# Performance work log

Measured on AMD Instinct MI355X. Metric: run time of the kernel, lower is better.

Reference implementation:

```python
import jax, jax.numpy as jnp
import numpy as np
from jax import lax

C, H, W = 512, 4, 4          # channel, height, width (size=[512,4,4])
SPLIT, PRED = 4, 4
WC = W // SPLIT              # width of each chunk = 1
L = C * H * WC               # lstm_size = 2048
B = 16


def setup_inputs() -> dict:
    key = jax.random.key(0)
    ks = jax.random.split(key, 12)
    s = 0.02  # ~1/sqrt(L), keeps gates in a sane range
    def w(k, shape):
        return jax.random.normal(k, shape, jnp.float32) * s
    return {
        "x1": jax.random.normal(ks[0], (B, C, H, W), jnp.float32),
        "x2": jax.random.normal(ks[1], (B, C, H, W), jnp.float32),
        "enc_Wih": w(ks[2], (2, 4 * L, L)),
        "enc_Whh": w(ks[3], (2, 4 * L, L)),
        "enc_bih": w(ks[4], (2, 4 * L)),
        "enc_bhh": w(ks[5], (2, 4 * L)),
        "dec_Wih": w(ks[6], (2, 4 * L, L)),
        "dec_Whh": w(ks[7], (2, 4 * L, L)),
        "dec_bih": w(ks[8], (2, 4 * L)),
        "dec_bhh": w(ks[9], (2, 4 * L)),
        "conv_W": w(ks[10], (C, 2 * C)),
        "conv_b": w(ks[11], (C,)),
    }


def _lstm2(x, state, Wih, Whh, bih, bhh):
    """One time-step of a 2-layer torch-style LSTM. x: [B, L]."""
    h, c = state  # each [2, B, L]
    hs, cs = [], []
    inp = x
    for l in range(2):
        g = inp @ Wih[l].T + bih[l] + h[l] @ Whh[l].T + bhh[l]  # [B, 4L]
        i, f, gg, o = jnp.split(g, 4, axis=-1)  # torch gate order i,f,g,o
        cn = jax.nn.sigmoid(f) * c[l] + jax.nn.sigmoid(i) * jnp.tanh(gg)
        hn = jax.nn.sigmoid(o) * jnp.tanh(cn)
        hs.append(hn); cs.append(cn)
        inp = hn
    return inp, (jnp.stack(hs), jnp.stack(cs))


def _split_chunks(x, reverse_inside=False):
    # torch.stack(torch.split(x, WC, dim=3)).view(SPLIT, -1, 1, L)
    b = x.shape[0]
    a = x.reshape(b, C, H, SPLIT, WC)
    if reverse_inside:
        a = a[..., ::-1]  # flip(dims=[4]) on the stacked chunks
    a = jnp.moveaxis(a, 3, 0)  # [SPLIT, B, C, H, WC]
    return a.reshape(SPLIT, b, L)


def _assemble(chunks, b, flip_inside=False):
    # chunks: [K, B, L] -> image block [B, C, H, K*WC] (width-concat order = chunk order)
    k = chunks.shape[0]
    a = chunks.reshape(k, b, C, H, WC)
    if flip_inside:
        a = a[..., ::-1]  # per-chunk flip(dims=[3]) in the torch code
    a = jnp.transpose(a, (1, 2, 3, 0, 4))
    return a.reshape(b, C, H, k * WC)


def _forward(x1, x2, enc_Wih, enc_Whh, enc_bih, enc_bhh,
             dec_Wih, dec_Whh, dec_bih, dec_bhh, conv_W, conv_b):
    b = x1.shape[0]
    z = jnp.zeros((2, b, L), x1.dtype)
    init = (z, z)

    def enc_step(st, x):
        out, st2 = _lstm2(x, st, enc_Wih, enc_Whh, enc_bih, enc_bhh)
        return st2, out

    def dec_step(st, x):
        out, st2 = _lstm2(x, st, dec_Wih, dec_Whh, dec_bih, dec_bhh)
        return st2, out

    def dec_ar(x0, st, n):
        def step(carry, _):
            x, s = carry
            out, s2 = _lstm2(x, s, dec_Wih, dec_Whh, dec_bih, dec_bhh)
            return (out, s2), out
        _, outs = lax.scan(step, (x0, st), None, length=n)
        return outs  # [n, B, L]

    x1_split = _split_chunks(x1)
    x1_split_rev = _split_chunks(x1, reverse_inside=True)
    x2_split = _split_chunks(x2)
    x2_split_rev = _split_chunks(x2, reverse_inside=True)

    # encoder: forward over x2 chunks; backward over internally-flipped x1 chunks
    hidden_x2, _ = lax.scan(enc_step, init, x2_split)
    hidden_x1r, _ = lax.scan(enc_step, init, x1_split_rev[::-1])

    st1, outs1 = lax.scan(dec_step, hidden_x2, x1_split)
    de1 = outs1[-1]
    preds1 = dec_ar(de1, st1, PRED + SPLIT - 1)  # 7 steps
    extra1 = _assemble(jnp.concatenate([de1[None], preds1], 0), b)
    x1_full = jnp.concatenate([x1, extra1], axis=3)  # width 3*W

    # decoder branch 2: consume reversed x2 chunks from hidden_x1r, prepend outputs
    st2, outs2 = lax.scan(dec_step, hidden_x1r, x2_split_rev[::-1])
    de2 = outs2[-1]
    preds2 = dec_ar(de2, st2, PRED + SPLIT - 1)
    # each output is prepended, so the last prediction ends up at the front
    extra2 = _assemble(jnp.concatenate([preds2[::-1], de2[None]], 0), b, flip_inside=True)
    x2_full = jnp.concatenate([extra2, x2], axis=3)

    x1_parts = (x1_full[..., :W], x1_full[..., W:-W], x1_full[..., -W:])
    x2_parts = (x2_full[..., :W], x2_full[..., W:-W], x2_full[..., -W:])

    mid = jnp.concatenate([x1_parts[1], x2_parts[1]], axis=1)  # [B, 2C, H, W]
    out = jnp.einsum('oi,bihw->bohw', conv_W, mid) + conv_b[None, :, None, None]
    out = jax.nn.leaky_relu(out, 0.2)  # make_layers: 1x1 conv + LeakyReLU
    return out, x1_parts, x2_parts


def reference(x1, x2, enc_Wih, enc_Whh, enc_bih, enc_bhh,
              dec_Wih, dec_Whh, dec_bih, dec_bhh, conv_W, conv_b):
    out, p1, p2 = _forward(x1, x2, enc_Wih, enc_Whh, enc_bih, enc_bhh,
                           dec_Wih, dec_Whh, dec_bih, dec_bhh, conv_W, conv_b)
    return (out,) + p1 + p2
```

## Files before the change

kernel.cpp:

```cpp
#include <hip/hip_runtime.h>
#include <cstdint>
#include <cstddef>


typedef __attribute__((ext_vector_type(8))) short short8;
typedef __attribute__((ext_vector_type(4))) short short4v;
typedef __attribute__((ext_vector_type(4))) float f32x4;

#define NBATCH 16
#define MAT_B   16777216ull
#define WSCALE  64.0f
#define INVWS   (1.0f / 64.0f)

__device__ __forceinline__ short f2bf(float f) {
    union { float f; unsigned u; } c; c.f = f;
    unsigned u = c.u;
    unsigned r = (u + 0x7FFFu + ((u >> 16) & 1u)) >> 16;
    return (short)r;
}

__device__ __forceinline__ uint32_t f4_to_fp8x4(float a, float b, float c, float d) {
    int p = __builtin_amdgcn_cvt_pk_fp8_f32(a, b, 0, false);
    p = __builtin_amdgcn_cvt_pk_fp8_f32(c, d, p, true);
    return (uint32_t)p;
}

__device__ __forceinline__ uint8_t f2fp8hw(float x) {
    return (uint8_t)(__builtin_amdgcn_cvt_pk_fp8_f32(x, x, 0, false) & 0xFF);
}

__device__ __forceinline__ float sigmoidf_(float x) { return 1.f / (1.f + __expf(-x)); }

__device__ __forceinline__ int apos(int n, int k) {
    return ((k >> 5) << 9) + ((((k >> 3) & 3) << 4) + n) * 8 + (k & 7);
}

__global__ __launch_bounds__(256) void k_pack8(
    const float* __restrict__ enc_Wih, const float* __restrict__ enc_Whh,
    const float* __restrict__ dec_Wih, const float* __restrict__ dec_Whh,
    uint8_t* __restrict__ dstbase)
{
    __shared__ uint8_t lbuf[16 * 1032];

    const int blk  = blockIdx.x;
    const int om   = blk >> 10;
    const int mat  = (om + 4) & 7;
    const int sub  = blk & 1023;
    const int bt   = sub >> 1;
    const int half = sub & 1;
    const int tid  = threadIdx.x;

    const float* srcs[4] = { enc_Wih, enc_Whh, dec_Wih, dec_Whh };
    const float* src = srcs[mat >> 1] + (size_t)(mat & 1) * 16777216ull;
    uint8_t* dst = dstbase + (size_t)mat * MAT_B
                 + (((size_t)bt * 64 + half * 32) << 9);

#pragma unroll 4
    for (int it = 0; it < 16; ++it) {
        int s  = it * 256 + tid;
        int rl = s >> 8;
        int c0 = (s & 255) * 4;
        int row = (rl >> 2) * 2048 + bt * 4 + (rl & 3);
        f32x4 v = __builtin_nontemporal_load(
            (const f32x4*)(src + (size_t)row * 2048 + half * 1024 + c0));
        uint32_t w32 = f4_to_fp8x4(v[0] * WSCALE, v[1] * WSCALE,
                                   v[2] * WSCALE, v[3] * WSCALE);
        *(uint32_t*)(lbuf + rl * 1032 + c0) = w32;
    }
    __syncthreads();

#pragma unroll 4
    for (int it = 0; it < 16; ++it) {
        int s    = it * 256 + tid;
        int fl   = s >> 7;
        int w    = s & 127;
        int lane = w >> 1;
        int j0   = (s & 1) * 4;
        int rl   = lane & 15;
        int c0   = fl * 32 + (lane >> 4) * 8 + j0;
        *(uint32_t*)(dst + (size_t)s * 4) = *(const uint32_t*)(lbuf + rl * 1032 + c0);
    }
}

__global__ __launch_bounds__(256) void k_init2(
    const float* __restrict__ x1, const float* __restrict__ x2,
    uint8_t* __restrict__ xc1, uint8_t* __restrict__ xc2,
    uint8_t* __restrict__ hbuf, float* __restrict__ cst,
    const float* __restrict__ Wc, short* __restrict__ Wcp,
    float* __restrict__ out)
{
    __shared__ short lb[16 * 1032];
    const int tid = threadIdx.x;

    if (blockIdx.x < 512) {
        int i = blockIdx.x * 256 + tid;
        cst[i] = 0.f;
        if (i < 65536) { hbuf[i] = 0; hbuf[131072 + i] = 0; }
        if (i < 32768) {
            int b = i >> 11, l = i & 2047;
            f32x4 v1 = ((const f32x4*)x1)[i];
            f32x4 v2 = ((const f32x4*)x2)[i];
            int p = apos(b, l);
            uint32_t q1 = f4_to_fp8x4(v1[0], v1[1], v1[2], v1[3]);
            uint32_t q2 = f4_to_fp8x4(v2[0], v2[1], v2[2], v2[3]);
#pragma unroll
            for (int s = 0; s < 4; ++s) {
                xc1[s * 32768 + p] = (uint8_t)(q1 >> (8 * s));
                xc2[s * 32768 + p] = (uint8_t)(q2 >> (8 * s));
            }
            ((f32x4*)(out + 131072))[i]     = v1;
            ((f32x4*)(out + 6 * 131072))[i] = v2;
        }
        return;
    }

    const int mt = blockIdx.x - 512;
#pragma unroll 4
    for (int it = 0; it < 16; ++it) {
        int s = it * 256 + tid;
        int rl = s >> 8;
        int c0 = (s & 255) * 4;
        f32x4 v = *(const f32x4*)(Wc + (size_t)(mt * 16 + rl) * 1024 + c0);
        short4v o;
        o[0] = f2bf(v[0]); o[1] = f2bf(v[1]); o[2] = f2bf(v[2]); o[3] = f2bf(v[3]);
        *(short4v*)(lb + rl * 1032 + c0) = o;
    }
    __syncthreads();
    short* dst = Wcp + (size_t)mt * 16384;
#pragma unroll 4
    for (int it = 0; it < 16; ++it) {
        int s    = it * 256 + tid;
        int fl   = s >> 7;
        int w    = s & 127;
        int lane = w >> 1;
        int j0   = (s & 1) * 4;
        int rl   = lane & 15;
        int c0   = fl * 32 + (lane >> 4) * 8 + j0;
        *(short4v*)(dst + (size_t)s * 4) = *(const short4v*)(lb + rl * 1032 + c0);
    }
}

struct CellJob {
    const uint8_t *Wih, *Whh;
    const float *bih, *bhh;
    const uint8_t *xA, *xB, *hin;
    float *cst;
    uint8_t *hout;
    float *svA, *svB;
    short *midp;
    int slot;
};

__global__ __launch_bounds__(512, 4) void k_cell(CellJob jA, CellJob jB)
{
    __shared__ float gpart[8][2][16][17];

    const CellJob& J = (blockIdx.x < 512) ? jA : jB;
    const int bt   = blockIdx.x & 511;
    const int tid  = threadIdx.x;
    const int w    = tid >> 6;
    const int lane = tid & 63;
    const int r    = lane & 15;
    const int g4   = lane >> 4;
    const int kq   = w & 3;

    const uint8_t* Wsrc = (w < 4) ? J.Wih : J.Whh;
    const uint8_t* uA   = (w < 4) ? J.xA : J.hin;
    const uint8_t* uB   = (w < 4) ? J.xB : (J.hin + 32768);

    const uint8_t* wp = Wsrc + (((size_t)bt * 64 + kq * 16) << 9) + lane * 8;
    const uint8_t* ap = uA + ((kq * 16) << 9) + lane * 8;
    const uint8_t* bp = uB + ((kq * 16) << 9) + lane * 8;

    long wreg[16];
#pragma unroll
    for (int i = 0; i < 16; ++i)
        wreg[i] = *(const long*)(wp + ((size_t)i << 9));

    f32x4 accA = {0.f, 0.f, 0.f, 0.f};
    f32x4 accB = {0.f, 0.f, 0.f, 0.f};
#pragma unroll
    for (int i = 0; i < 16; ++i) {
        long av = *(const long*)(ap + ((size_t)i << 9));
        long bv = *(const long*)(bp + ((size_t)i << 9));
        accA = __builtin_amdgcn_mfma_f32_16x16x32_fp8_fp8(wreg[i], av, accA, 0, 0, 0);
        accB = __builtin_amdgcn_mfma_f32_16x16x32_fp8_fp8(wreg[i], bv, accB, 0, 0, 0);
    }

#pragma unroll
    for (int q = 0; q < 4; ++q) {
        gpart[w][0][g4 * 4 + q][r] = accA[q];
        gpart[w][1][g4 * 4 + q][r] = accB[q];
    }
    __syncthreads();

    if (tid < 128) {
        const int br  = tid >> 6;
        const int chl = (tid >> 4) & 3;
        const int n   = tid & 15;

        float gi = 0.f, gf = 0.f, gg = 0.f, go = 0.f;
#pragma unroll
        for (int ww = 0; ww < 8; ++ww) {
            gi += gpart[ww][br][chl][n];
            gf += gpart[ww][br][4 + chl][n];
            gg += gpart[ww][br][8 + chl][n];
            go += gpart[ww][br][12 + chl][n];
        }
        const int ch = bt * 4 + chl;
        gi = gi * INVWS + J.bih[ch]            + J.bhh[ch];
        gf = gf * INVWS + J.bih[2048 + ch]     + J.bhh[2048 + ch];
        gg = gg * INVWS + J.bih[2 * 2048 + ch] + J.bhh[2 * 2048 + ch];
        go = go * INVWS + J.bih[3 * 2048 + ch] + J.bhh[3 * 2048 + ch];

        const size_t idx = ((size_t)br * NBATCH + n) * 2048 + ch;
        float cold = J.cst[idx];
        float cn = sigmoidf_(gf) * cold + sigmoidf_(gi) * tanhf(gg);
        float hn = sigmoidf_(go) * tanhf(cn);
        J.cst[idx] = cn;
        J.hout[br * 32768 + apos(n, ch)] = f2fp8hw(hn);
        if (br == 0) { if (J.svA) J.svA[(size_t)n * 2048 + ch] = hn; }
        else         { if (J.svB) J.svB[(size_t)n * 2048 + ch] = hn; }
        if (J.midp) {
            int i8, pos;
            if (br == 0) { i8 = ch >> 2;         pos = n * 16 + (ch & 3) * 4 + J.slot; }
            else         { i8 = 512 + (ch >> 2); pos = n * 16 + (ch & 3) * 4 + (3 - J.slot); }
            J.midp[(pos >> 4) * 16384 + (i8 >> 5) * 512
                   + (((i8 >> 3) & 3) * 16 + (pos & 15)) * 8 + (i8 & 7)] = f2bf(hn);
        }
    }
}

__global__ __launch_bounds__(512) void k_fin2(
    const short* __restrict__ Wcp, const short* __restrict__ midp,
    const float* __restrict__ bc,
    const float* __restrict__ SA, const float* __restrict__ SB,
    float* __restrict__ out)
{
    __shared__ float gp[4][16][17];
    const int tid = threadIdx.x;

    if (blockIdx.x < 256) {
        int i  = blockIdx.x * 512 + tid;
        int q  = i >> 15;
        int rr = i & 32767;
        const float* base = (q < 2) ? SA : SB;
        int sl0 = (q == 0) ? 0 : (q == 1) ? 4 : (q == 2) ? 7 : 3;
        int stp = (q < 2) ? 1 : -1;
        f32x4 o;
#pragma unroll
        for (int w2 = 0; w2 < 4; ++w2)
            o[w2] = base[(size_t)(sl0 + stp * w2) * 32768 + rr];
        ((f32x4*)(out + (size_t)(2 + q) * 131072))[rr] = o;
        return;
    }

    const int blk2 = blockIdx.x - 256;
    const int mt = blk2 >> 4, nt = blk2 & 15;
    if (tid < 256) {
        const int kw = tid >> 6, lane = tid & 63;
        const short* ap = Wcp + (size_t)mt * 16384 + kw * 8 * 512 + lane * 8;
        const short* bp = midp + (size_t)nt * 16384 + kw * 8 * 512 + lane * 8;
        f32x4 acc = {0.f, 0.f, 0.f, 0.f};
#pragma unroll
        for (int i = 0; i < 8; ++i) {
            short8 a = *(const short8*)(ap + i * 512);
            short8 b = *(const short8*)(bp + i * 512);
            acc = __builtin_amdgcn_mfma_f32_16x16x32_bf16(a, b, acc, 0, 0, 0);
        }
        const int r = lane & 15, g4 = lane >> 4;
#pragma unroll
        for (int q = 0; q < 4; ++q) gp[kw][g4 * 4 + q][r] = acc[q];
    }
    __syncthreads();
    if (tid < 256) {
        const int m = tid >> 4, nl = tid & 15;
        float s = gp[0][m][nl] + gp[1][m][nl] + gp[2][m][nl] + gp[3][m][nl];
        const int o = mt * 16 + m, pos = nt * 16 + nl;
        s += bc[o];
        s = s > 0.f ? s : 0.2f * s;
        const int b = pos >> 4, hp = (pos >> 2) & 3, w = pos & 3;
        out[(size_t)b * 8192 + o * 16 + hp * 4 + w] = s;
    }
}

__global__ void k_wsfail(float* out) { if (threadIdx.x == 0 && blockIdx.x == 0) out[0] = -7.7e7f; }

extern "C" void kernel_launch(void* const* d_in, const int* in_sizes, int n_in,
                              void* d_out, int out_size, void* d_ws, size_t ws_size,
                              hipStream_t stream)
{
    const float* x1      = (const float*)d_in[0];
    const float* x2      = (const float*)d_in[1];
    const float* enc_Wih = (const float*)d_in[2];
    const float* enc_Whh = (const float*)d_in[3];
    const float* enc_bih = (const float*)d_in[4];
    const float* enc_bhh = (const float*)d_in[5];
    const float* dec_Wih = (const float*)d_in[6];
    const float* dec_Whh = (const float*)d_in[7];
    const float* dec_bih = (const float*)d_in[8];
    const float* dec_bhh = (const float*)d_in[9];
    const float* conv_W  = (const float*)d_in[10];
    const float* conv_b  = (const float*)d_in[11];
    float* out = (float*)d_out;

    uint8_t* Wb   = (uint8_t*)d_ws;
    uint8_t* xc1  = Wb + 8 * MAT_B;
    uint8_t* xc2  = xc1 + 131072;
    uint8_t* hbuf = xc2 + 131072;
    float*   cst  = (float*)(hbuf + 262144);
    float*   SA   = cst + 131072;
    float*   SB   = SA + 262144;
    short*   midp = (short*)(SB + 262144);
    short*   Wcp  = midp + 262144;
    size_t need = (size_t)((char*)(Wcp + 524288) - (char*)d_ws);
    if (ws_size < need) { k_wsfail<<<1, 64, 0, stream>>>(out); return; }

    k_init2<<<544, 256, 0, stream>>>(x1, x2, xc1, xc2, hbuf, cst, conv_W, Wcp, out);
    k_pack8<<<8192, 256, 0, stream>>>(enc_Wih, enc_Whh, dec_Wih, dec_Whh, Wb);

    auto hB = [&](int layer, int par) -> uint8_t* {
        return hbuf + layer * 131072 + par * 65536;
    };

    auto mkJob = [&](int t, int layer) -> CellJob {
        const bool enc = (t <= 4);
        CellJob j;
        int base = enc ? 0 : 4;
        j.Wih = Wb + (size_t)(base + layer) * MAT_B;
        j.Whh = Wb + (size_t)(base + 2 + layer) * MAT_B;
        j.bih = (enc ? enc_bih : dec_bih) + layer * 8192;
        j.bhh = (enc ? enc_bhh : dec_bhh) + layer * 8192;
        if (layer == 0) {
            if (t <= 4)      { j.xA = xc2 + (size_t)(t - 1) * 32768; j.xB = xc1 + (size_t)(4 - t) * 32768; }
            else if (t <= 8) { j.xA = xc1 + (size_t)(t - 5) * 32768; j.xB = xc2 + (size_t)(8 - t) * 32768; }
            else             { const uint8_t* hp = hB(1, (t - 1) & 1); j.xA = hp; j.xB = hp + 32768; }
            j.hin = hB(0, (t - 1) & 1);
            j.cst = cst;
            j.hout = hB(0, t & 1);
            j.svA = nullptr; j.svB = nullptr; j.midp = nullptr; j.slot = 0;
        } else {
            const uint8_t* hx = hB(0, t & 1);
            j.xA = hx; j.xB = hx + 32768;
            j.hin = hB(1, (t - 1) & 1);
            j.cst = cst + 65536;
            j.hout = hB(1, t & 1);
            j.svA = (t >= 8) ? SA + (size_t)(t - 8) * 32768 : nullptr;
            j.svB = (t >= 8) ? SB + (size_t)(t - 8) * 32768 : nullptr;
            j.midp = (t >= 8 && t <= 11) ? midp : nullptr;
            j.slot = (t >= 8) ? (t - 8) : 0;
        }
        return j;
    };

    k_cell<<<512, 512, 0, stream>>>(mkJob(1, 0), mkJob(1, 0));
    for (int t = 2; t <= 8; ++t)
        k_cell<<<1024, 512, 0, stream>>>(mkJob(t, 0), mkJob(t - 1, 1));
    k_cell<<<512, 512, 0, stream>>>(mkJob(8, 1), mkJob(8, 1));
    for (int t = 9; t <= 15; ++t) {
        k_cell<<<512, 512, 0, stream>>>(mkJob(t, 0), mkJob(t, 0));
        k_cell<<<512, 512, 0, stream>>>(mkJob(t, 1), mkJob(t, 1));
    }

    k_fin2<<<768, 512, 0, stream>>>(Wcp, midp, conv_b, SA, SB, out);
}
```

Measured before the change: 372.7 us.

## Merge init and weight-pack kernels, skip zero-state work at first step

```diff
diff --git a/kernel.cpp b/kernel.cpp
--- a/kernel.cpp
+++ b/kernel.cpp
@@ -6,6 +6,7 @@
 typedef __attribute__((ext_vector_type(8))) short short8;
 typedef __attribute__((ext_vector_type(4))) short short4v;
 typedef __attribute__((ext_vector_type(4))) float f32x4;
+typedef __attribute__((ext_vector_type(2))) unsigned long long u64x2;
 
 #define NBATCH 16
 #define MAT_B   16777216ull
@@ -35,42 +36,94 @@
     return ((k >> 5) << 9) + ((((k >> 3) & 3) << 4) + n) * 8 + (k & 7);
 }
 
-__global__ __launch_bounds__(256) void k_pack8(
+__global__ __launch_bounds__(256) void k_pack8i(
     const float* __restrict__ enc_Wih, const float* __restrict__ enc_Whh,
     const float* __restrict__ dec_Wih, const float* __restrict__ dec_Whh,
-    uint8_t* __restrict__ dstbase)
+    uint8_t* __restrict__ dstbase,
+    const float* __restrict__ x1, const float* __restrict__ x2,
+    uint8_t* __restrict__ xc1, uint8_t* __restrict__ xc2,
+    const float* __restrict__ Wc, short* __restrict__ Wcp,
+    float* __restrict__ out)
 {
-    __shared__ uint8_t lbuf[16 * 1032];
-
-    const int blk  = blockIdx.x;
-    const int om   = blk >> 10;
-    const int mat  = (om + 4) & 7;
-    const int sub  = blk & 1023;
-    const int bt   = sub >> 1;
-    const int half = sub & 1;
-    const int tid  = threadIdx.x;
-
-    const float* srcs[4] = { enc_Wih, enc_Whh, dec_Wih, dec_Whh };
-    const float* src = srcs[mat >> 1] + (size_t)(mat & 1) * 16777216ull;
-    uint8_t* dst = dstbase + (size_t)mat * MAT_B
-                 + (((size_t)bt * 64 + half * 32) << 9);
+    __shared__ uint8_t lbuf[16 * 1040];
+    const int blk = blockIdx.x;
+    const int tid = threadIdx.x;
+
+    if (blk < 8192) {
+        const int om   = blk >> 10;
+        const int mat  = (om + 4) & 7;
+        const int sub  = blk & 1023;
+        const int bt   = sub >> 1;
+        const int half = sub & 1;
+
+        const float* srcs[4] = { enc_Wih, enc_Whh, dec_Wih, dec_Whh };
+        const float* src = srcs[mat >> 1] + (size_t)(mat & 1) * 16777216ull;
+        uint8_t* dst = dstbase + (size_t)mat * MAT_B
+                     + (((size_t)bt * 64 + half * 32) << 9);
 
 #pragma unroll 4
-    for (int it = 0; it < 16; ++it) {
+        for (int it = 0; it < 16; ++it) {
+            int s  = it * 256 + tid;
+            int rl = s >> 8;
+            int c0 = (s & 255) * 4;
+            int row = (rl >> 2) * 2048 + bt * 4 + (rl & 3);
+            f32x4 v = __builtin_nontemporal_load(
+                (const f32x4*)(src + (size_t)row * 2048 + half * 1024 + c0));
+            uint32_t w32 = f4_to_fp8x4(v[0] * WSCALE, v[1] * WSCALE,
+                                       v[2] * WSCALE, v[3] * WSCALE);
+            *(uint32_t*)(lbuf + rl * 1032 + c0) = w32;
+        }
+        __syncthreads();
+
+#pragma unroll
+        for (int it = 0; it < 4; ++it) {
+            int s  = it * 256 + tid;
+            int fl = s >> 5;
+            int m  = s & 31;
+            const uint8_t* p0 = lbuf + ((2 * m) & 15) * 1032 + fl * 32 + (m >> 3) * 8;
+            u64x2 v;
+            v[0] = *(const unsigned long long*)p0;
+            v[1] = *(const unsigned long long*)(p0 + 1032);
+            *(u64x2*)(dst + (size_t)s * 16) = v;
+        }
+        return;
+    }
+
+    if (blk < 8320) {
+        int i = (blk - 8192) * 256 + tid;
+        int b = i >> 11, l = i & 2047;
+        f32x4 v1 = ((const f32x4*)x1)[i];
+        f32x4 v2 = ((const f32x4*)x2)[i];
+        int p = apos(b, l);
+        uint32_t q1 = f4_to_fp8x4(v1[0], v1[1], v1[2], v1[3]);
+        uint32_t q2 = f4_to_fp8x4(v2[0], v2[1], v2[2], v2[3]);
+#pragma unroll
+        for (int s = 0; s < 4; ++s) {
+            xc1[s * 32768 + p] = (uint8_t)(q1 >> (8 * s));
+            xc2[s * 32768 + p] = (uint8_t)(q2 >> (8 * s));
+        }
+        ((f32x4*)(out + 131072))[i]     = v1;
+        ((f32x4*)(out + 6 * 131072))[i] = v2;
+        return;
+    }
+
+    short* lb16 = (short*)lbuf;
+    const int mt2 = blk - 8320;
+    const int mt = mt2 >> 1, h = mt2 & 1;
+#pragma unroll 4
+    for (int it = 0; it < 8; ++it) {
         int s  = it * 256 + tid;
-        int rl = s >> 8;
-        int c0 = (s & 255) * 4;
-        int row = (rl >> 2) * 2048 + bt * 4 + (rl & 3);
-        f32x4 v = __builtin_nontemporal_load(
-            (const f32x4*)(src + (size_t)row * 2048 + half * 1024 + c0));
-        uint32_t w32 = f4_to_fp8x4(v[0] * WSCALE, v[1] * WSCALE,
-                                   v[2] * WSCALE, v[3] * WSCALE);
-        *(uint32_t*)(lbuf + rl * 1032 + c0) = w32;
+        int rl = s >> 7;
+        int c0 = (s & 127) * 4;
+        f32x4 v = *(const f32x4*)(Wc + (size_t)(mt * 16 + rl) * 1024 + h * 512 + c0);
+        short4v o;
+        o[0] = f2bf(v[0]); o[1] = f2bf(v[1]); o[2] = f2bf(v[2]); o[3] = f2bf(v[3]);
+        *(short4v*)(lb16 + rl * 520 + c0) = o;
     }
     __syncthreads();
-
+    short* dst = Wcp + (size_t)mt * 16384 + h * 8192;
 #pragma unroll 4
-    for (int it = 0; it < 16; ++it) {
+    for (int it = 0; it < 8; ++it) {
         int s    = it * 256 + tid;
         int fl   = s >> 7;
         int w    = s & 127;
@@ -78,65 +131,7 @@
         int j0   = (s & 1) * 4;
         int rl   = lane & 15;
         int c0   = fl * 32 + (lane >> 4) * 8 + j0;
-        *(uint32_t*)(dst + (size_t)s * 4) = *(const uint32_t*)(lbuf + rl * 1032 + c0);
-    }
-}
-
-__global__ __launch_bounds__(256) void k_init2(
-    const float* __restrict__ x1, const float* __restrict__ x2,
-    uint8_t* __restrict__ xc1, uint8_t* __restrict__ xc2,
-    uint8_t* __restrict__ hbuf, float* __restrict__ cst,
-    const float* __restrict__ Wc, short* __restrict__ Wcp,
-    float* __restrict__ out)
-{
-    __shared__ short lb[16 * 1032];
-    const int tid = threadIdx.x;
-
-    if (blockIdx.x < 512) {
-        int i = blockIdx.x * 256 + tid;
-        cst[i] = 0.f;
-        if (i < 65536) { hbuf[i] = 0; hbuf[131072 + i] = 0; }
-        if (i < 32768) {
-            int b = i >> 11, l = i & 2047;
-            f32x4 v1 = ((const f32x4*)x1)[i];
-            f32x4 v2 = ((const f32x4*)x2)[i];
-            int p = apos(b, l);
-            uint32_t q1 = f4_to_fp8x4(v1[0], v1[1], v1[2], v1[3]);
-            uint32_t q2 = f4_to_fp8x4(v2[0], v2[1], v2[2], v2[3]);
-#pragma unroll
-            for (int s = 0; s < 4; ++s) {
-                xc1[s * 32768 + p] = (uint8_t)(q1 >> (8 * s));
-                xc2[s * 32768 + p] = (uint8_t)(q2 >> (8 * s));
-            }
-            ((f32x4*)(out + 131072))[i]     = v1;
-            ((f32x4*)(out + 6 * 131072))[i] = v2;
-        }
-        return;
-    }
-
-    const int mt = blockIdx.x - 512;
-#pragma unroll 4
-    for (int it = 0; it < 16; ++it) {
-        int s = it * 256 + tid;
-        int rl = s >> 8;
-        int c0 = (s & 255) * 4;
-        f32x4 v = *(const f32x4*)(Wc + (size_t)(mt * 16 + rl) * 1024 + c0);
-        short4v o;
-        o[0] = f2bf(v[0]); o[1] = f2bf(v[1]); o[2] = f2bf(v[2]); o[3] = f2bf(v[3]);
-        *(short4v*)(lb + rl * 1032 + c0) = o;
-    }
-    __syncthreads();
-    short* dst = Wcp + (size_t)mt * 16384;
-#pragma unroll 4
-    for (int it = 0; it < 16; ++it) {
-        int s    = it * 256 + tid;
-        int fl   = s >> 7;
-        int w    = s & 127;
-        int lane = w >> 1;
-        int j0   = (s & 1) * 4;
-        int rl   = lane & 15;
-        int c0   = fl * 32 + (lane >> 4) * 8 + j0;
-        *(short4v*)(dst + (size_t)s * 4) = *(const short4v*)(lb + rl * 1032 + c0);
+        *(short4v*)(dst + (size_t)s * 4) = *(const short4v*)(lb16 + rl * 520 + c0);
     }
 }
 
@@ -149,6 +144,7 @@
     float *svA, *svB;
     short *midp;
     int slot;
+    int zf;
 };
 
 __global__ __launch_bounds__(512, 4) void k_cell(CellJob jA, CellJob jB)
@@ -164,27 +160,31 @@
     const int g4   = lane >> 4;
     const int kq   = w & 3;
 
-    const uint8_t* Wsrc = (w < 4) ? J.Wih : J.Whh;
-    const uint8_t* uA   = (w < 4) ? J.xA : J.hin;
-    const uint8_t* uB   = (w < 4) ? J.xB : (J.hin + 32768);
-
-    const uint8_t* wp = Wsrc + (((size_t)bt * 64 + kq * 16) << 9) + lane * 8;
-    const uint8_t* ap = uA + ((kq * 16) << 9) + lane * 8;
-    const uint8_t* bp = uB + ((kq * 16) << 9) + lane * 8;
-
-    long wreg[16];
-#pragma unroll
-    for (int i = 0; i < 16; ++i)
-        wreg[i] = *(const long*)(wp + ((size_t)i << 9));
-
     f32x4 accA = {0.f, 0.f, 0.f, 0.f};
     f32x4 accB = {0.f, 0.f, 0.f, 0.f};
-#pragma unroll
-    for (int i = 0; i < 16; ++i) {
-        long av = *(const long*)(ap + ((size_t)i << 9));
-        long bv = *(const long*)(bp + ((size_t)i << 9));
-        accA = __builtin_amdgcn_mfma_f32_16x16x32_fp8_fp8(wreg[i], av, accA, 0, 0, 0);
-        accB = __builtin_amdgcn_mfma_f32_16x16x32_fp8_fp8(wreg[i], bv, accB, 0, 0, 0);
+
+    const bool skip = (J.zf & 1) && (w >= 4);
+    if (!skip) {
+        const uint8_t* Wsrc = (w < 4) ? J.Wih : J.Whh;
+        const uint8_t* uA   = (w < 4) ? J.xA : J.hin;
+        const uint8_t* uB   = (w < 4) ? J.xB : (J.hin + 32768);
+
+        const uint8_t* wp = Wsrc + (((size_t)bt * 64 + kq * 16) << 9) + lane * 8;
+        const uint8_t* ap = uA + ((kq * 16) << 9) + lane * 8;
+        const uint8_t* bp = uB + ((kq * 16) << 9) + lane * 8;
+
+        long wreg[16];
+#pragma unroll
+        for (int i = 0; i < 16; ++i)
+            wreg[i] = *(const long*)(wp + ((size_t)i << 9));
+
+#pragma unroll
+        for (int i = 0; i < 16; ++i) {
+            long av = *(const long*)(ap + ((size_t)i << 9));
+            long bv = *(const long*)(bp + ((size_t)i << 9));
+            accA = __builtin_amdgcn_mfma_f32_16x16x32_fp8_fp8(wreg[i], av, accA, 0, 0, 0);
+            accB = __builtin_amdgcn_mfma_f32_16x16x32_fp8_fp8(wreg[i], bv, accB, 0, 0, 0);
+        }
     }
 
 #pragma unroll
@@ -214,7 +214,7 @@
         go = go * INVWS + J.bih[3 * 2048 + ch] + J.bhh[3 * 2048 + ch];
 
         const size_t idx = ((size_t)br * NBATCH + n) * 2048 + ch;
-        float cold = J.cst[idx];
+        float cold = (J.zf & 2) ? 0.f : J.cst[idx];
         float cn = sigmoidf_(gf) * cold + sigmoidf_(gi) * tanhf(gg);
         float hn = sigmoidf_(go) * tanhf(cn);
         J.cst[idx] = cn;
@@ -316,8 +316,8 @@
     size_t need = (size_t)((char*)(Wcp + 524288) - (char*)d_ws);
     if (ws_size < need) { k_wsfail<<<1, 64, 0, stream>>>(out); return; }
 
-    k_init2<<<544, 256, 0, stream>>>(x1, x2, xc1, xc2, hbuf, cst, conv_W, Wcp, out);
-    k_pack8<<<8192, 256, 0, stream>>>(enc_Wih, enc_Whh, dec_Wih, dec_Whh, Wb);
+    k_pack8i<<<8384, 256, 0, stream>>>(enc_Wih, enc_Whh, dec_Wih, dec_Whh, Wb,
+                                       x1, x2, xc1, xc2, conv_W, Wcp, out);
 
     auto hB = [&](int layer, int par) -> uint8_t* {
         return hbuf + layer * 131072 + par * 65536;
@@ -331,6 +331,7 @@
         j.Whh = Wb + (size_t)(base + 2 + layer) * MAT_B;
         j.bih = (enc ? enc_bih : dec_bih) + layer * 8192;
         j.bhh = (enc ? enc_bhh : dec_bhh) + layer * 8192;
+        j.zf = (t == 1) ? 3 : 0;
         if (layer == 0) {
             if (t <= 4)      { j.xA = xc2 + (size_t)(t - 1) * 32768; j.xB = xc1 + (size_t)(4 - t) * 32768; }
             else if (t <= 8) { j.xA = xc1 + (size_t)(t - 5) * 32768; j.xB = xc2 + (size_t)(8 - t) * 32768; }
```

New measurement: 365.7 us. Within noise of the previous version (-1.9%).
